# Optimization experiments

Hardware: AMD Instinct MI355X
Metric: run time of the kernel (lower is better)

## Reference

```python
import jax, jax.numpy as jnp
import numpy as np

B, N1, N2, D, E = 8, 1024, 256, 16, 16


def setup_inputs() -> dict:
    key = jax.random.key(0)
    ks = jax.random.split(key, 11)
    stdv = 1.0 / np.sqrt(E)
    u = lambda k, shape: jax.random.uniform(k, shape, jnp.float32, -stdv, stdv)
    inputs = jax.random.normal(ks[0], (B, N1, N2, D), dtype=jnp.float32)
    # adjacency matrices (dense, nonnegative); scaled for numerical sanity
    adj0 = jax.random.uniform(ks[1], (N1, N1), dtype=jnp.float32) / np.float32(np.sqrt(N1))
    adj1 = jax.random.uniform(ks[2], (N2, N2), dtype=jnp.float32) / np.float32(np.sqrt(N2))
    return {
        "inputs": inputs, "adj0": adj0, "adj1": adj1,
        "W": u(ks[3], (D, E)), "b": u(ks[4], (E,)),
        "W_s0": u(ks[5], (D, E)), "b_s0": u(ks[6], (E,)),
        "W_s1": u(ks[7], (D, E)), "b_s1": u(ks[8], (E,)),
        "W_s01": u(ks[9], (D, E)), "b_s01": u(ks[10], (E,)),
    }


def _helper(x, adj_modes, W, b):
    # TGCNHelper: mode-wise adjacency products along the given tensor modes,
    # then a linear projection on the feature axis.
    h = x
    for mode, A in adj_modes:
        if mode == 0:
            h = jnp.einsum('bijd,ik->bkjd', h, A)  # mode-0 (n1) aggregation
        else:
            h = jnp.einsum('bijd,jk->bikd', h, A)  # mode-1 (n2) aggregation
    return jnp.einsum('bijd,de->bije', h, W) + b


def reference(inputs, adj0, adj1, W, b, W_s0, b_s0, W_s1, b_s1, W_s01, b_s01):
    # dense mode-product branch: inputs x_{-1} W + bias
    h_lin = jnp.einsum('bijd,de->bije', inputs, W) + b
    # subsets of valid_modes [0,1]: {0}, {1}, {0,1}
    h0 = _helper(inputs, [(0, adj0)], W_s0, b_s0)
    h1 = _helper(inputs, [(1, adj1)], W_s1, b_s1)
    h01 = _helper(inputs, [(0, adj0), (1, adj1)], W_s01, b_s01)
    # stack + sum over last dim == direct sum; then ReLU
    return jax.nn.relu(h_lin + h0 + h1 + h01)
```

## Files before the change

kernel.cpp:

```cpp
#include <hip/hip_runtime.h>

#define BB  8
#define NN1 1024
#define NN2 256
#define DD  16
#define EE  16
#define NCOL (NN2 * DD)
#define SLPB 2

using bf16x8  = __attribute__((ext_vector_type(8))) short;
using f32x4   = __attribute__((ext_vector_type(4))) float;
using ushort8 = __attribute__((ext_vector_type(8))) unsigned short;

__device__ __forceinline__ ushort f2bf(float x) {
  unsigned u = __float_as_uint(x);
  unsigned r = (u + 0x7FFFu + ((u >> 16) & 1u)) >> 16;
  return (ushort)r;
}
__device__ __forceinline__ float bf2f(ushort u) {
  return __uint_as_float((unsigned)u << 16);
}
__device__ __forceinline__ unsigned pkbf(float a, float b) {
  return (unsigned)f2bf(a) | ((unsigned)f2bf(b) << 16);
}

#define GLDS16(g, l)                                                       \
  __builtin_amdgcn_global_load_lds(                                        \
      (const __attribute__((address_space(1))) void*)(g),                  \
      (__attribute__((address_space(3))) void*)(l), 16, 0, 0)

__global__ __launch_bounds__(256)
void k_prep(const float* __restrict__ src, ushort* __restrict__ dst,
            int nr, int kd, size_t srcBatch, size_t dstBatch, int ps) {
  __shared__ float tile[64][65];
  const int t = threadIdx.x;
  const int r0 = blockIdx.x * 64;
  const int k0 = blockIdx.y * 64;
  const float* s = src + (size_t)blockIdx.z * srcBatch;
  ushort* d = dst + (size_t)blockIdx.z * dstBatch;

#pragma unroll
  for (int it = 0; it < 4; ++it) {
    const int kr = it * 16 + (t >> 4);
    const int rc = (t & 15) * 4;
    float4 v = *reinterpret_cast<const float4*>(&s[(size_t)(k0 + kr) * nr + r0 + rc]);
    tile[kr][rc] = v.x; tile[kr][rc + 1] = v.y;
    tile[kr][rc + 2] = v.z; tile[kr][rc + 3] = v.w;
  }
  __syncthreads();

#pragma unroll
  for (int pass = 0; pass < 2; ++pass) {
    const int task = t + pass * 256;
    const int pr = task >> 3;
    const int gl = task & 7;
    const int r = r0 + pr;
    int klb;
    if (ps) {
      klb = (gl ^ (r & 7)) * 8;
    } else {
      const int f = (r >> 1) & 3;
      klb = (gl >> 2) * 32 + ((gl & 3) ^ f) * 8;
    }
    unsigned w[4];
#pragma unroll
    for (int e2 = 0; e2 < 4; ++e2)
      w[e2] = pkbf(tile[klb + e2 * 2][pr], tile[klb + e2 * 2 + 1][pr]);
    *reinterpret_cast<uint4*>(&d[(size_t)r * kd + k0 + gl * 8]) =
        *reinterpret_cast<const uint4*>(w);
  }
}

__global__ __launch_bounds__(1024)
void k_mode0_mfma(const ushort* __restrict__ At, const ushort* __restrict__ Xt,
                  ushort* __restrict__ Y) {
  __shared__ ushort As[2][16384];
  __shared__ ushort Bs[2][16384];

  const int t = threadIdx.x;
  const int lane = t & 63;
  const int wid = t >> 6;
  const int wr = wid >> 2;
  const int wc = wid & 3;

  const int nwg = (int)gridDim.x;
  const int wg  = (int)blockIdx.x;
  const int orig = (wg & 7) * (nwg >> 3) + (wg >> 3);
  const int b  = orig >> 6;
  const int rem = orig & 63;
  const int c0 = (rem >> 2) << 8;
  const int p0 = (rem & 3) << 8;

  const ushort* Bb = Xt + (size_t)b * (NCOL * 1024);

  f32x4 acc[4][4];
#pragma unroll
  for (int i = 0; i < 4; ++i)
#pragma unroll
    for (int j = 0; j < 4; ++j) acc[i][j] = (f32x4)0.f;

  const int lm = lane & 15, g = lane >> 4;

  const int ksx0 = (g ^ (lm & 7)) << 3;
  const int ksx1 = ksx0 ^ 32;
  int aoff[4], boff[4];
#pragma unroll
  for (int f = 0; f < 4; ++f) {
    aoff[f] = (wr * 64 + f * 16 + lm) * 64;
    boff[f] = (wc * 64 + f * 16 + lm) * 64;
  }

#define STG_A(buf, kt, h) do {                                             \
    const int rs_ = ((wid >> 2) << 6) + (h) * 32 + ((wid & 3) << 3);       \
    GLDS16(At + (size_t)(p0 + rs_ + (lane >> 3)) * 1024 + (kt) * 64 +      \
               (lane & 7) * 8, &As[buf][rs_ * 64]);                        \
  } while (0)

#define STG_B(buf, kt, h) do {                                             \
    const int rs_ = ((wid >> 2) << 6) + (h) * 32 + ((wid & 3) << 3);       \
    GLDS16(Bb + (size_t)(c0 + rs_ + (lane >> 3)) * 1024 + (kt) * 64 +      \
               (lane & 7) * 8, &Bs[buf][rs_ * 64]);                        \
  } while (0)

#define VM3 asm volatile("s_waitcnt vmcnt(3)" ::: "memory")
#define VM2 asm volatile("s_waitcnt vmcnt(2)" ::: "memory")
#define VM1 asm volatile("s_waitcnt vmcnt(1)" ::: "memory")
#define VM0 asm volatile("s_waitcnt vmcnt(0)" ::: "memory")
#define NOWAIT ((void)0)
#define NOSTG  ((void)0)

#define PHASE(buf, qi, qj, STGSTMT, WAITSTMT) do {                         \
    STGSTMT;                                                               \
    WAITSTMT;                                                              \
    __builtin_amdgcn_s_barrier();                                          \
    __builtin_amdgcn_sched_barrier(0);                                     \
    bf16x8 a00 = *reinterpret_cast<const bf16x8*>(&As[buf][aoff[(qi)*2+0] + ksx0]); \
    bf16x8 a10 = *reinterpret_cast<const bf16x8*>(&As[buf][aoff[(qi)*2+1] + ksx0]); \
    bf16x8 b00 = *reinterpret_cast<const bf16x8*>(&Bs[buf][boff[(qj)*2+0] + ksx0]); \
    bf16x8 b10 = *reinterpret_cast<const bf16x8*>(&Bs[buf][boff[(qj)*2+1] + ksx0]); \
    bf16x8 a01 = *reinterpret_cast<const bf16x8*>(&As[buf][aoff[(qi)*2+0] + ksx1]); \
    bf16x8 a11 = *reinterpret_cast<const bf16x8*>(&As[buf][aoff[(qi)*2+1] + ksx1]); \
    bf16x8 b01 = *reinterpret_cast<const bf16x8*>(&Bs[buf][boff[(qj)*2+0] + ksx1]); \
    bf16x8 b11 = *reinterpret_cast<const bf16x8*>(&Bs[buf][boff[(qj)*2+1] + ksx1]); \
    __builtin_amdgcn_s_setprio(1);                                         \
    acc[(qi)*2+0][(qj)*2+0] = __builtin_amdgcn_mfma_f32_16x16x32_bf16(a00, b00, acc[(qi)*2+0][(qj)*2+0], 0, 0, 0); \
    acc[(qi)*2+0][(qj)*2+1] = __builtin_amdgcn_mfma_f32_16x16x32_bf16(a00, b10, acc[(qi)*2+0][(qj)*2+1], 0, 0, 0); \
    acc[(qi)*2+1][(qj)*2+0] = __builtin_amdgcn_mfma_f32_16x16x32_bf16(a10, b00, acc[(qi)*2+1][(qj)*2+0], 0, 0, 0); \
    acc[(qi)*2+1][(qj)*2+1] = __builtin_amdgcn_mfma_f32_16x16x32_bf16(a10, b10, acc[(qi)*2+1][(qj)*2+1], 0, 0, 0); \
    acc[(qi)*2+0][(qj)*2+0] = __builtin_amdgcn_mfma_f32_16x16x32_bf16(a01, b01, acc[(qi)*2+0][(qj)*2+0], 0, 0, 0); \
    acc[(qi)*2+0][(qj)*2+1] = __builtin_amdgcn_mfma_f32_16x16x32_bf16(a01, b11, acc[(qi)*2+0][(qj)*2+1], 0, 0, 0); \
    acc[(qi)*2+1][(qj)*2+0] = __builtin_amdgcn_mfma_f32_16x16x32_bf16(a11, b01, acc[(qi)*2+1][(qj)*2+0], 0, 0, 0); \
    acc[(qi)*2+1][(qj)*2+1] = __builtin_amdgcn_mfma_f32_16x16x32_bf16(a11, b11, acc[(qi)*2+1][(qj)*2+1], 0, 0, 0); \
    __builtin_amdgcn_s_setprio(0);                                         \
  } while (0)

  STG_A(0, 0, 0); STG_B(0, 0, 0); STG_A(0, 0, 1); STG_B(0, 0, 1);

  for (int it = 0; it < 8; ++it) {
    const int t1 = 2 * it + 1, t2 = 2 * it + 2;
    PHASE(0, 0, 0, STG_A(1, t1, 0), VM3);
    PHASE(0, 1, 0, STG_B(1, t1, 0), VM3);
    PHASE(0, 0, 1, STG_A(1, t1, 1), VM3);
    PHASE(0, 1, 1, STG_B(1, t1, 1), NOWAIT);
    __builtin_amdgcn_s_barrier();
    if (it < 7) {
      PHASE(1, 0, 0, STG_A(0, t2, 0), VM3);
      PHASE(1, 1, 0, STG_B(0, t2, 0), VM3);
      PHASE(1, 0, 1, STG_A(0, t2, 1), VM3);
      PHASE(1, 1, 1, STG_B(0, t2, 1), NOWAIT);
    } else {
      PHASE(1, 0, 0, NOSTG, VM2);
      PHASE(1, 1, 0, NOSTG, VM1);
      PHASE(1, 0, 1, NOSTG, VM0);
      PHASE(1, 1, 1, NOSTG, NOWAIT);
    }
    __builtin_amdgcn_s_barrier();
  }
#undef PHASE
#undef STG_A
#undef STG_B

  ushort* Yb = Y + (size_t)b * ((size_t)NN1 * NCOL);
  const int orow = g * 4;
#pragma unroll
  for (int i = 0; i < 4; ++i)
#pragma unroll
    for (int j = 0; j < 4; ++j) {
      const int p = p0 + wr * 64 + i * 16 + orow;
      const int c = c0 + wc * 64 + j * 16 + lm;
      ushort* dst = Yb + (size_t)p * NCOL + c;
#pragma unroll
      for (int e = 0; e < 4; ++e) dst[(size_t)e * NCOL] = f2bf(acc[i][j][e]);
    }
}

__global__ __launch_bounds__(512)
void k_pm(const float* __restrict__ x, const ushort* __restrict__ y0,
          const ushort* __restrict__ A1t,
          const float* __restrict__ W,   const float* __restrict__ bW,
          const float* __restrict__ W0,  const float* __restrict__ b0,
          const float* __restrict__ W1,  const float* __restrict__ b1,
          const float* __restrict__ W01, const float* __restrict__ b01,
          float* __restrict__ out) {
  __shared__ ushort As[2][8192];
  __shared__ ushort St[8][SLPB * 16][32];

  const int t = threadIdx.x;
  const int lane = t & 63;
  const int wid = t >> 6;
  const int lm = lane & 15, g = lane >> 4;
  const int wq  = wid >> 1;
  const int wmi = wid & 1;
  const size_t sl0 = (size_t)blockIdx.x * SLPB;

  {
    const size_t base = (sl0 * NCOL) + (size_t)t * DD;
    const float4 x0 = *reinterpret_cast<const float4*>(&x[base]);
    const float4 x1 = *reinterpret_cast<const float4*>(&x[base + 4]);
    const float4 x2 = *reinterpret_cast<const float4*>(&x[base + 8]);
    const float4 x3 = *reinterpret_cast<const float4*>(&x[base + 12]);
    const uint4 yv0 = *reinterpret_cast<const uint4*>(&y0[base]);
    const uint4 yv1 = *reinterpret_cast<const uint4*>(&y0[base + 8]);
    unsigned xw0[4] = {pkbf(x0.x, x0.y), pkbf(x0.z, x0.w), pkbf(x1.x, x1.y), pkbf(x1.z, x1.w)};
    unsigned xw1[4] = {pkbf(x2.x, x2.y), pkbf(x2.z, x2.w), pkbf(x3.x, x3.y), pkbf(x3.z, x3.w)};
    *reinterpret_cast<uint4*>(&As[0][t * 16])     = *reinterpret_cast<const uint4*>(xw0);
    *reinterpret_cast<uint4*>(&As[0][t * 16 + 8]) = *reinterpret_cast<const uint4*>(xw1);
    *reinterpret_cast<uint4*>(&As[1][t * 16])     = yv0;
    *reinterpret_cast<uint4*>(&As[1][t * 16 + 8]) = yv1;
  }

  bf16x8 wfr, wfs;
#pragma unroll
  for (int jj = 0; jj < 8; ++jj) {
    const int k = g * 8 + jj;
    const float vr = (k < 16) ? W[k * 16 + lm]  : W0[(k - 16) * 16 + lm];
    const float vs = (k < 16) ? W1[k * 16 + lm] : W01[(k - 16) * 16 + lm];
    wfr[jj] = (short)f2bf(vr);
    wfs[jj] = (short)f2bf(vs);
  }
  const float bias = bW[lm] + b0[lm] + b1[lm] + b01[lm];

  __syncthreads();

  f32x4 acc[4];
#pragma unroll
  for (int i = 0; i < 4; ++i) {
    const int grp = wmi * 16 + wq * 4 + i;
    const int row = grp * 16 + lm;
    bf16x8 a;
    if (g < 2)
      a = *reinterpret_cast<const bf16x8*>(&As[0][row * 16 + g * 8]);
    else
      a = *reinterpret_cast<const bf16x8*>(&As[1][row * 16 + (g - 2) * 8]);

    f32x4 cb; cb[0] = bias; cb[1] = bias; cb[2] = bias; cb[3] = bias;
    acc[i] = __builtin_amdgcn_mfma_f32_16x16x32_bf16(a, wfr, cb, 0, 0, 0);
    const f32x4 sD = __builtin_amdgcn_mfma_f32_16x16x32_bf16(a, wfs, (f32x4)0.f, 0, 0, 0);

    const int m = wmi * 16 + lm;
    const int kc = wq * 2 + (i >> 1);
    const int chunkL = ((i & 1) << 1) + (g >> 1);
    const int phys = chunkL ^ ((m >> 1) & 3);
    unsigned pw[2] = {pkbf(sD[0], sD[1]), pkbf(sD[2], sD[3])};
    *reinterpret_cast<uint2*>(&St[kc][m][phys * 8 + (g & 1) * 4]) =
        *reinterpret_cast<const uint2*>(pw);
  }

  __syncthreads();

  const int srow = wid * 32 + (lane >> 2);
  const int schk = (lane & 3) * 8;

#define STAGEA(buf, kc)                                                    \
  do {                                                                     \
    GLDS16(A1t + (size_t)srow * 256 + (kc) * 32 + schk,                    \
           &As[buf][(wid * 32) * 32]);                                     \
    GLDS16(A1t + (size_t)(srow + 16) * 256 + (kc) * 32 + schk,             \
           &As[buf][(wid * 32 + 16) * 32]);                                \
  } while (0)

  int aro[4];
#pragma unroll
  for (int f = 0; f < 4; ++f) {
    const int ra = wq * 64 + f * 16 + lm;
    aro[f] = ra * 32 + ((g ^ ((ra >> 1) & 3)) << 3);
  }
  const int rwB = wmi * 16 + lm;
  const int bofs = (rwB * 32) + ((g ^ ((rwB >> 1) & 3)) << 3);

  STAGEA(0, 0);
  int cur = 0;
  for (int kc = 0; kc < 8; ++kc) {
    if (kc < 7) {
      STAGEA(cur ^ 1, kc + 1);
      asm volatile("s_waitcnt vmcnt(2)" ::: "memory");
    } else {
      asm volatile("s_waitcnt vmcnt(0)" ::: "memory");
    }
    __builtin_amdgcn_s_barrier();
    __builtin_amdgcn_sched_barrier(0);

    bf16x8 af[4];
#pragma unroll
    for (int f = 0; f < 4; ++f)
      af[f] = *reinterpret_cast<const bf16x8*>(&As[cur][aro[f]]);
    const bf16x8 bfr = *reinterpret_cast<const bf16x8*>(&St[kc][0][0] + bofs);

#pragma unroll
    for (int i = 0; i < 4; ++i)
      acc[i] = __builtin_amdgcn_mfma_f32_16x16x32_bf16(af[i], bfr, acc[i], 0, 0, 0);

    __builtin_amdgcn_sched_barrier(0);
    __builtin_amdgcn_s_barrier();
    cur ^= 1;
  }
#undef STAGEA

  float* os = out + (sl0 + wmi) * NCOL;
#pragma unroll
  for (int i = 0; i < 4; ++i) {
    const int qb = wq * 64 + i * 16 + g * 4;
#pragma unroll
    for (int rr = 0; rr < 4; ++rr)
      os[(size_t)(qb + rr) * EE + lm] = fmaxf(acc[i][rr], 0.f);
  }
}

extern "C" void kernel_launch(void* const* d_in, const int* in_sizes, int n_in,
                              void* d_out, int out_size, void* d_ws, size_t ws_size,
                              hipStream_t stream) {
  const float* x    = (const float*)d_in[0];
  const float* adj0 = (const float*)d_in[1];
  const float* adj1 = (const float*)d_in[2];
  const float* W    = (const float*)d_in[3];
  const float* bW   = (const float*)d_in[4];
  const float* Ws0  = (const float*)d_in[5];
  const float* bs0  = (const float*)d_in[6];
  const float* Ws1  = (const float*)d_in[7];
  const float* bs1  = (const float*)d_in[8];
  const float* Ws01 = (const float*)d_in[9];
  const float* bs01 = (const float*)d_in[10];
  float* out = (float*)d_out;

  const size_t SLICE = (size_t)NN1 * NCOL;
  const size_t AT_B  = (size_t)1024 * 1024 * 2;
  const size_t A1T_B = (size_t)256 * 256 * 2;
  const size_t XT_B  = (size_t)NCOL * 1024 * 2;
  const size_t Y0_B  = SLICE * 2;
  const size_t HEAD  = AT_B + A1T_B;
  const size_t PER_B = XT_B + Y0_B;

  int nb_max = (int)((ws_size > HEAD ? ws_size - HEAD : 0) / PER_B);
  if (nb_max > BB) nb_max = BB;
  if (nb_max < 1)  nb_max = 1;

  ushort* At  = (ushort*)d_ws;
  ushort* A1t = (ushort*)((char*)d_ws + AT_B);
  ushort* Xt  = (ushort*)((char*)d_ws + HEAD);
  ushort* y0  = (ushort*)((char*)d_ws + HEAD + (size_t)nb_max * XT_B);

  k_prep<<<dim3(16, 16, 1), 256, 0, stream>>>(adj0, At, 1024, 1024, 0, 0, 1);
  k_prep<<<dim3(4, 4, 1), 256, 0, stream>>>(adj1, A1t, 256, 256, 0, 0, 0);

  for (int c0 = 0; c0 < BB; c0 += nb_max) {
    const int nb = (BB - c0 < nb_max) ? (BB - c0) : nb_max;
    const float* xc = x   + (size_t)c0 * SLICE;
    float*       oc = out + (size_t)c0 * SLICE;

    k_prep<<<dim3(NCOL / 64, 16, nb), 256, 0, stream>>>(
        xc, Xt, NCOL, 1024, SLICE, (size_t)NCOL * 1024, 1);

    dim3 g1(nb * 64);
    k_mode0_mfma<<<g1, 1024, 0, stream>>>(At, Xt, y0);

    dim3 g2(nb * NN1 / SLPB);
    k_pm<<<g2, 512, 0, stream>>>(xc, y0, A1t, W, bW, Ws0, bs0,
                                 Ws1, bs1, Ws01, bs01, oc);
  }
}
```

Before: 199.4 us.

## Widen k_pm adjacency staging to 64-wide K tiles with padded shared layout

Restructures the mode-1 stage of k_pm. The adjacency is now staged in 64-column K tiles (4 iterations instead of 8), which halves the number of barrier pairs and uses a new XOR swizzle over 8 chunks. The x/y0 input tile is stored as interleaved 40-element padded rows, so each lane does one uniform LDS load instead of branching between two buffers. MFMA issue is wrapped in s_setprio, and the A1t prep flag is flipped so its layout matches the new staging. Shared memory per block grows, which could reduce occupancy, and correctness depends on the prep flag change matching the new swizzle.

```diff
diff --git a/kernel.cpp b/kernel.cpp
--- a/kernel.cpp
+++ b/kernel.cpp
@@ -202,8 +202,10 @@
           const float* __restrict__ W1,  const float* __restrict__ b1,
           const float* __restrict__ W01, const float* __restrict__ b01,
           float* __restrict__ out) {
-  __shared__ ushort As[2][8192];
-  __shared__ ushort St[8][SLPB * 16][32];
+  __shared__ ushort SH[40960];
+  ushort* xy  = SH;
+  ushort* Asb = SH;
+  ushort* Stp = SH + 32768;
 
   const int t = threadIdx.x;
   const int lane = t & 63;
@@ -223,10 +225,11 @@
     const uint4 yv1 = *reinterpret_cast<const uint4*>(&y0[base + 8]);
     unsigned xw0[4] = {pkbf(x0.x, x0.y), pkbf(x0.z, x0.w), pkbf(x1.x, x1.y), pkbf(x1.z, x1.w)};
     unsigned xw1[4] = {pkbf(x2.x, x2.y), pkbf(x2.z, x2.w), pkbf(x3.x, x3.y), pkbf(x3.z, x3.w)};
-    *reinterpret_cast<uint4*>(&As[0][t * 16])     = *reinterpret_cast<const uint4*>(xw0);
-    *reinterpret_cast<uint4*>(&As[0][t * 16 + 8]) = *reinterpret_cast<const uint4*>(xw1);
-    *reinterpret_cast<uint4*>(&As[1][t * 16])     = yv0;
-    *reinterpret_cast<uint4*>(&As[1][t * 16 + 8]) = yv1;
+    ushort* row = xy + t * 40;
+    *reinterpret_cast<uint4*>(row)      = *reinterpret_cast<const uint4*>(xw0);
+    *reinterpret_cast<uint4*>(row + 8)  = *reinterpret_cast<const uint4*>(xw1);
+    *reinterpret_cast<uint4*>(row + 16) = yv0;
+    *reinterpret_cast<uint4*>(row + 24) = yv1;
   }
 
   bf16x8 wfr, wfs;
@@ -247,11 +250,7 @@
   for (int i = 0; i < 4; ++i) {
     const int grp = wmi * 16 + wq * 4 + i;
     const int row = grp * 16 + lm;
-    bf16x8 a;
-    if (g < 2)
-      a = *reinterpret_cast<const bf16x8*>(&As[0][row * 16 + g * 8]);
-    else
-      a = *reinterpret_cast<const bf16x8*>(&As[1][row * 16 + (g - 2) * 8]);
+    const bf16x8 a = *reinterpret_cast<const bf16x8*>(&xy[row * 40 + g * 8]);
 
     f32x4 cb; cb[0] = bias; cb[1] = bias; cb[2] = bias; cb[3] = bias;
     acc[i] = __builtin_amdgcn_mfma_f32_16x16x32_bf16(a, wfr, cb, 0, 0, 0);
@@ -262,53 +261,60 @@
     const int chunkL = ((i & 1) << 1) + (g >> 1);
     const int phys = chunkL ^ ((m >> 1) & 3);
     unsigned pw[2] = {pkbf(sD[0], sD[1]), pkbf(sD[2], sD[3])};
-    *reinterpret_cast<uint2*>(&St[kc][m][phys * 8 + (g & 1) * 4]) =
+    *reinterpret_cast<uint2*>(&Stp[kc * 1024 + m * 32 + phys * 8 + (g & 1) * 4]) =
         *reinterpret_cast<const uint2*>(pw);
   }
 
   __syncthreads();
 
-  const int srow = wid * 32 + (lane >> 2);
-  const int schk = (lane & 3) * 8;
-
-#define STAGEA(buf, kc)                                                    \
+#define STAGEA(buf, kt)                                                    \
   do {                                                                     \
-    GLDS16(A1t + (size_t)srow * 256 + (kc) * 32 + schk,                    \
-           &As[buf][(wid * 32) * 32]);                                     \
-    GLDS16(A1t + (size_t)(srow + 16) * 256 + (kc) * 32 + schk,             \
-           &As[buf][(wid * 32 + 16) * 32]);                                \
+    _Pragma("unroll")                                                      \
+    for (int is = 0; is < 4; ++is) {                                       \
+      const int rowbase = wid * 32 + is * 8;                               \
+      GLDS16(A1t + (size_t)(rowbase + (lane >> 3)) * 256 + (kt) * 64 +     \
+                 (lane & 7) * 8,                                           \
+             Asb + (buf) * 16384 + rowbase * 64);                          \
+    }                                                                      \
   } while (0)
 
-  int aro[4];
+  int aro[4][2];
 #pragma unroll
   for (int f = 0; f < 4; ++f) {
     const int ra = wq * 64 + f * 16 + lm;
-    aro[f] = ra * 32 + ((g ^ ((ra >> 1) & 3)) << 3);
+#pragma unroll
+    for (int ks = 0; ks < 2; ++ks)
+      aro[f][ks] = ra * 64 + (((ks * 4 + g) ^ (ra & 7)) << 3);
   }
   const int rwB = wmi * 16 + lm;
   const int bofs = (rwB * 32) + ((g ^ ((rwB >> 1) & 3)) << 3);
 
   STAGEA(0, 0);
   int cur = 0;
-  for (int kc = 0; kc < 8; ++kc) {
-    if (kc < 7) {
-      STAGEA(cur ^ 1, kc + 1);
-      asm volatile("s_waitcnt vmcnt(2)" ::: "memory");
+  for (int kt = 0; kt < 4; ++kt) {
+    if (kt < 3) {
+      STAGEA(cur ^ 1, kt + 1);
+      asm volatile("s_waitcnt vmcnt(4)" ::: "memory");
     } else {
       asm volatile("s_waitcnt vmcnt(0)" ::: "memory");
     }
     __builtin_amdgcn_s_barrier();
     __builtin_amdgcn_sched_barrier(0);
 
-    bf16x8 af[4];
-#pragma unroll
-    for (int f = 0; f < 4; ++f)
-      af[f] = *reinterpret_cast<const bf16x8*>(&As[cur][aro[f]]);
-    const bf16x8 bfr = *reinterpret_cast<const bf16x8*>(&St[kc][0][0] + bofs);
-
-#pragma unroll
-    for (int i = 0; i < 4; ++i)
-      acc[i] = __builtin_amdgcn_mfma_f32_16x16x32_bf16(af[i], bfr, acc[i], 0, 0, 0);
+#pragma unroll
+    for (int ks = 0; ks < 2; ++ks) {
+      const int kc = kt * 2 + ks;
+      bf16x8 af[4];
+#pragma unroll
+      for (int f = 0; f < 4; ++f)
+        af[f] = *reinterpret_cast<const bf16x8*>(&Asb[cur * 16384 + aro[f][ks]]);
+      const bf16x8 bfr = *reinterpret_cast<const bf16x8*>(&Stp[kc * 1024 + bofs]);
+      __builtin_amdgcn_s_setprio(1);
+#pragma unroll
+      for (int i = 0; i < 4; ++i)
+        acc[i] = __builtin_amdgcn_mfma_f32_16x16x32_bf16(af[i], bfr, acc[i], 0, 0, 0);
+      __builtin_amdgcn_s_setprio(0);
+    }
 
     __builtin_amdgcn_sched_barrier(0);
     __builtin_amdgcn_s_barrier();
@@ -360,7 +366,7 @@
   ushort* y0  = (ushort*)((char*)d_ws + HEAD + (size_t)nb_max * XT_B);
 
   k_prep<<<dim3(16, 16, 1), 256, 0, stream>>>(adj0, At, 1024, 1024, 0, 0, 1);
-  k_prep<<<dim3(4, 4, 1), 256, 0, stream>>>(adj1, A1t, 256, 256, 0, 0, 0);
+  k_prep<<<dim3(4, 4, 1), 256, 0, stream>>>(adj1, A1t, 256, 256, 0, 0, 1);
 
   for (int c0 = 0; c0 < BB; c0 += nb_max) {
     const int nb = (BB - c0 < nb_max) ? (BB - c0) : nb_max;
```

Measured after the change: 193.5 us, median of 3. -2.9%, faster.
